# Kernel optimization log

Hardware: AMD Instinct MI355X
Metric: run time of the kernel (lower is better)

Reference implementation:

```python
import jax, jax.numpy as jnp
import numpy as np
import math

N0 = 50000      # nodes at level 0
E0 = 800000     # edges at level 0 (fixed edge buffer, masked when pooled)
D = 128         # hidden_dim == latent_dim
L = 2           # args.mpl_layers
NB = 2          # args.num_blocks (SAGEConvs per block)
RATIO = 0.5     # args.mpl_ratio
EPS = 1e-12


def setup_inputs() -> dict:
    key = jax.random.key(0)
    ks = jax.random.split(key, 6)
    x = jax.random.normal(ks[0], (N0, D), jnp.float32)
    edge_index = jax.random.randint(ks[1], (2, E0), 0, N0, jnp.int32)
    n_convs = (2 * L + 1) * NB  # down(4) + bottom(2) + up(4) = 10
    Wl = jax.random.normal(ks[2], (n_convs, D, D), jnp.float32) * 0.05
    bl = jax.random.normal(ks[3], (n_convs, D), jnp.float32) * 0.05
    Wr = jax.random.normal(ks[4], (n_convs, D, D), jnp.float32) * 0.05
    pool_p = jax.random.normal(ks[5], (L, D), jnp.float32)
    return {"x": x, "edge_index": edge_index, "Wl": Wl, "bl": bl, "Wr": Wr,
            "pool_p": pool_p}


def _sage(x, src, dst, valid, W_l, b_l, W_r, n):
    """PyG SAGEConv (mean aggr): lin_l(mean_{j->i} x_j) + lin_r(x_i).
    Invalid (masked) edges contribute neither to the sum nor the count."""
    msg = x[src] * valid[:, None]                       # [E, D]
    s = jax.ops.segment_sum(msg, dst, num_segments=n)   # [n, D]
    cnt = jax.ops.segment_sum(valid, dst, num_segments=n)
    mean = s / jnp.maximum(cnt, 1.0)[:, None]
    return mean @ W_l.T + b_l + x @ W_r.T


def _cal_ew(w, src, dst, valid, n):
    """WeightedEdgeConv.cal_ew (no_grad in original)."""
    deg = jax.ops.segment_sum(valid, src, num_segments=n)
    normed = w / jnp.where(deg > 0, deg, 1.0)
    w_send = normed[src] * valid
    aggr_w = jax.ops.segment_sum(w_send, dst, num_segments=n) + EPS
    ec = w_send / aggr_w[dst]
    return jax.lax.stop_gradient(ec), jax.lax.stop_gradient(aggr_w)


def _econv(x, src, dst, ec, n, aggregating=True):
    """WeightedEdgeConv.forward: gather -> scale by edge weight -> scatter-add."""
    if aggregating:
        return jax.ops.segment_sum(x[src] * ec[:, None], dst, num_segments=n)
    return jax.ops.segment_sum(x[dst] * ec[:, None], src, num_segments=n)


def reference(x, edge_index, Wl, bl, Wr, pool_p):
    src, dst = edge_index[0], edge_index[1]
    valid = jnp.ones((E0,), x.dtype)
    n = N0
    conv = 0
    down_outs, down_edges, ecs, perms, sizes = [], [], [], [], []
    w = jnp.ones((N0,), x.dtype)  # b_data.weights (ones by default)

    # ---- down path ----
    for l in range(L):
        for _ in range(NB):
            x = _sage(x, src, dst, valid, Wl[conv], bl[conv], Wr[conv], n)
            conv += 1
        down_outs.append(x)
        down_edges.append((src, dst, valid))
        sizes.append(n)
        ec, w = _cal_ew(w, src, dst, valid, n)
        ecs.append(ec)
        x = _econv(x, src, dst, ec, n, aggregating=True)
        # TopKPooling: score = x.p/||p||, keep top ceil(ratio*n), gate by tanh
        p = pool_p[l]
        score = x @ p / jnp.linalg.norm(p)
        k = int(math.ceil(RATIO * n))
        vals, perm = jax.lax.top_k(score, k)
        x = x[perm] * jnp.tanh(vals)[:, None]
        w = w[perm]
        new_id = jnp.full((n,), -1, jnp.int32).at[perm].set(
            jnp.arange(k, dtype=jnp.int32))
        src2, dst2 = new_id[src], new_id[dst]
        keep = ((src2 >= 0) & (dst2 >= 0)).astype(x.dtype)
        valid = valid * keep
        src = jnp.maximum(src2, 0)
        dst = jnp.maximum(dst2, 0)
        perms.append(perm)
        n = k

    # ---- bottom ----
    for _ in range(NB):
        x = _sage(x, src, dst, valid, Wl[conv], bl[conv], Wr[conv], n)
        conv += 1

    # ---- up path ----
    for i in range(L):
        u = L - 1 - i
        src, dst, valid = down_edges[u]
        n = sizes[u]
        # Unpool: scatter into zeros at kept-node indices
        x = jnp.zeros((n, x.shape[-1]), x.dtype).at[perms[u]].set(x)
        x = _econv(x, src, dst, ecs[u], n, aggregating=False)
        for _ in range(NB):
            x = _sage(x, src, dst, valid, Wl[conv], bl[conv], Wr[conv], n)
            conv += 1
        x = x + down_outs[u]  # skip connection
    return x
```

## Files before the change

kernel.cpp:

```cpp
#include <hip/hip_runtime.h>
#include <stdint.h>

#define DEV __device__ __forceinline__

constexpr int N0 = 50000;
constexpr int E0 = 800000;
constexpr int D  = 128;

typedef __attribute__((ext_vector_type(8))) short bf16x8;
typedef __attribute__((ext_vector_type(4))) float f32x4;

DEV float bf2f(unsigned u) { return __uint_as_float(u << 16); }
DEV unsigned short f2bf(float f) {
  unsigned u = __float_as_uint(f);
  unsigned r = u + 0x7fffu + ((u >> 16) & 1u);
  return (unsigned short)(r >> 16);
}

DEV unsigned wave_incl_scan(unsigned v, int lane) {
  #pragma unroll
  for (int off = 1; off < 64; off <<= 1) {
    unsigned u = __shfl_up(v, (unsigned)off);
    if (lane >= off) v += u;
  }
  return v;
}

__global__ void k_count(const int* __restrict__ src, const int* __restrict__ dst,
                        unsigned* cnt_src, unsigned* cnt_dst,
                        unsigned* __restrict__ rank_src, unsigned* __restrict__ rank_dst) {
  int e = blockIdx.x * blockDim.x + threadIdx.x;
  if (e < E0) {
    rank_src[e] = atomicAdd(&cnt_src[src[e]], 1u);
    rank_dst[e] = atomicAdd(&cnt_dst[dst[e]], 1u);
  }
}

__global__ void k_psum(const unsigned* __restrict__ in, int n, unsigned* __restrict__ part) {
  int t = threadIdx.x, lane = t & 63, w = t >> 6;
  int base = blockIdx.x * 1024 + t * 4;
  unsigned s = 0;
  #pragma unroll
  for (int j = 0; j < 4; ++j) { int i = base + j; if (i < n) s += in[i]; }
  #pragma unroll
  for (int off = 32; off >= 1; off >>= 1) s += __shfl_xor(s, off);
  __shared__ unsigned ws[4];
  if (lane == 0) ws[w] = s;
  __syncthreads();
  if (t == 0) part[blockIdx.x] = ws[0] + ws[1] + ws[2] + ws[3];
}

__global__ void k_scoff(const unsigned* __restrict__ part, int nch,
                        unsigned* __restrict__ off, unsigned* __restrict__ total_out) {
  if (threadIdx.x == 0) {
    unsigned run = 0;
    for (int c = 0; c < nch; ++c) { off[c] = run; run += part[c]; }
    *total_out = run;
  }
}

__global__ void k_sapply(const unsigned* __restrict__ in, const unsigned* __restrict__ choff,
                         int n, unsigned* __restrict__ out) {
  int t = threadIdx.x, lane = t & 63, w = t >> 6;
  int base = blockIdx.x * 1024 + t * 4;
  unsigned v[4]; unsigned s = 0;
  #pragma unroll
  for (int j = 0; j < 4; ++j) { int i = base + j; v[j] = (i < n) ? in[i] : 0u; s += v[j]; }
  unsigned incl = wave_incl_scan(s, lane);
  __shared__ unsigned wsum[4], woff[4];
  if (lane == 63) wsum[w] = incl;
  __syncthreads();
  if (t == 0) { unsigned run = 0; for (int j = 0; j < 4; ++j) { woff[j] = run; run += wsum[j]; } }
  __syncthreads();
  unsigned run = choff[blockIdx.x] + woff[w] + incl - s;
  #pragma unroll
  for (int j = 0; j < 4; ++j) {
    int i = base + j;
    if (i < n) out[i] = run;
    run += v[j];
  }
}

__global__ void k_fill2(const int* __restrict__ src, const int* __restrict__ dst,
                        const unsigned* __restrict__ rank_src, const unsigned* __restrict__ rank_dst,
                        const unsigned* __restrict__ indptr_src, const unsigned* __restrict__ indptr_dst,
                        int* __restrict__ adj_src, int* __restrict__ adj_dst) {
  int e = blockIdx.x * blockDim.x + threadIdx.x;
  if (e < E0) {
    int s = src[e], d = dst[e];
    adj_dst[indptr_dst[d] + rank_dst[e]] = s;
    adj_src[indptr_src[s] + rank_src[e]] = d;
  }
}

__global__ void k_adj_next2(const int* __restrict__ adjd, const int* __restrict__ adjs,
                            const int* __restrict__ new_id,
                            int* __restrict__ outd, int* __restrict__ outs) {
  int pos = blockIdx.x * blockDim.x + threadIdx.x;
  if (pos < E0) {
    int a = adjd[pos];
    outd[pos] = (a >= 0) ? new_id[a] : -1;
    int b = adjs[pos];
    outs[pos] = (b >= 0) ? new_id[b] : -1;
  }
}

__global__ void k_adj_next(const int* __restrict__ adj_prev, const int* __restrict__ new_id,
                           int* __restrict__ adj_out) {
  int pos = blockIdx.x * blockDim.x + threadIdx.x;
  if (pos < E0) {
    int a = adj_prev[pos];
    adj_out[pos] = (a >= 0) ? new_id[a] : -1;
  }
}

__global__ void k_wt_pk3(const float* __restrict__ Wl, const float* __restrict__ Wr,
                         unsigned short* __restrict__ Bh, unsigned short* __restrict__ Bm,
                         unsigned short* __restrict__ Bl) {
  int idx = blockIdx.x * blockDim.x + threadIdx.x;
  if (idx >= 10 * 8 * 8 * 64) return;
  int l  = idx & 63;
  int ct = (idx >> 6) & 7;
  int ks = (idx >> 9) & 7;
  int c  = idx >> 12;
  int k0 = ks * 32 + (l >> 4) * 8;
  int o  = ct * 16 + (l & 15);
  const float* Wrow = (k0 < 128) ? (Wl + ((size_t)c * 128 + o) * 128 + k0)
                                 : (Wr + ((size_t)c * 128 + o) * 128 + (k0 - 128));
  size_t base = (size_t)idx * 8;
  #pragma unroll
  for (int j = 0; j < 8; ++j) {
    float wv = Wrow[j];
    unsigned short h = f2bf(wv);
    float r1 = wv - bf2f(h);
    unsigned short m = f2bf(r1);
    float r2 = r1 - bf2f(m);
    Bh[base + j] = h;
    Bm[base + j] = m;
    Bl[base + j] = f2bf(r2);
  }
}

template<bool MEAN, bool MASKED, bool ECW>
__global__ void k_gf32(const float* __restrict__ x, const int* __restrict__ adj,
                       const float* __restrict__ ecs, const unsigned* __restrict__ indptr,
                       const int* __restrict__ orig, int n, float* __restrict__ out) {
  int wid = (blockIdx.x * blockDim.x + threadIdx.x) >> 6;
  int lane = threadIdx.x & 63;
  if (wid >= n) return;
  int o = orig ? orig[wid] : wid;
  unsigned s0 = indptr[o], s1 = indptr[o + 1];
  int half = lane >> 5, sl = lane & 31;
  float a0 = 0.f, a1 = 0.f, a2 = 0.f, a3 = 0.f, cnt = 0.f;
  for (unsigned idx = s0; idx < s1; idx += 8) {
    #pragma unroll
    for (int j = 0; j < 4; ++j) {
      unsigned e = idx + j * 2 + half;
      if (e < s1) {
        int a = adj[e];
        if (!MASKED || a >= 0) {
          const float4 v = *(const float4*)(x + (size_t)a * D + sl * 4);
          if (ECW) {
            float w = ecs[e];
            a0 = fmaf(w, v.x, a0); a1 = fmaf(w, v.y, a1);
            a2 = fmaf(w, v.z, a2); a3 = fmaf(w, v.w, a3);
          } else {
            a0 += v.x; a1 += v.y; a2 += v.z; a3 += v.w;
          }
          cnt += 1.f;
        }
      }
    }
  }
  a0 += __shfl_xor(a0, 32); a1 += __shfl_xor(a1, 32);
  a2 += __shfl_xor(a2, 32); a3 += __shfl_xor(a3, 32);
  if (MEAN) {
    cnt += __shfl_xor(cnt, 32);
    if (!MASKED) cnt = (float)(s1 - s0);
    float inv = 1.0f / fmaxf(cnt, 1.0f);
    a0 *= inv; a1 *= inv; a2 *= inv; a3 *= inv;
  }
  if (half == 0)
    *(float4*)(out + (size_t)wid * D + sl * 4) = make_float4(a0, a1, a2, a3);
}

template<bool MEAN, bool MASKED, bool ECW>
__global__ void k_gbf(const unsigned* __restrict__ xb, const int* __restrict__ adj,
                      const float* __restrict__ ecs, const unsigned* __restrict__ indptr,
                      const int* __restrict__ orig, int n,
                      float* __restrict__ out, unsigned* __restrict__ outbf) {
  int wid = (blockIdx.x * blockDim.x + threadIdx.x) >> 6;
  int lane = threadIdx.x & 63;
  if (wid >= n) return;
  int o = orig ? orig[wid] : wid;
  unsigned s0 = indptr[o], s1 = indptr[o + 1];
  int q = lane >> 4, sl = lane & 15;
  float acc[8];
  #pragma unroll
  for (int k = 0; k < 8; ++k) acc[k] = 0.f;
  float cnt = 0.f;
  for (unsigned idx = s0; idx < s1; idx += 16) {
    #pragma unroll
    for (int j = 0; j < 4; ++j) {
      unsigned e = idx + j * 4 + q;
      if (e < s1) {
        int a = adj[e];
        if (!MASKED || a >= 0) {
          const uint4 v = *(const uint4*)(xb + (size_t)a * 64 + sl * 4);
          float f0 = bf2f(v.x & 0xffffu), f1 = bf2f(v.x >> 16);
          float f2 = bf2f(v.y & 0xffffu), f3 = bf2f(v.y >> 16);
          float f4 = bf2f(v.z & 0xffffu), f5 = bf2f(v.z >> 16);
          float f6 = bf2f(v.w & 0xffffu), f7 = bf2f(v.w >> 16);
          if (ECW) {
            float w = ecs[e];
            acc[0] = fmaf(w, f0, acc[0]); acc[1] = fmaf(w, f1, acc[1]);
            acc[2] = fmaf(w, f2, acc[2]); acc[3] = fmaf(w, f3, acc[3]);
            acc[4] = fmaf(w, f4, acc[4]); acc[5] = fmaf(w, f5, acc[5]);
            acc[6] = fmaf(w, f6, acc[6]); acc[7] = fmaf(w, f7, acc[7]);
          } else {
            acc[0] += f0; acc[1] += f1; acc[2] += f2; acc[3] += f3;
            acc[4] += f4; acc[5] += f5; acc[6] += f6; acc[7] += f7;
          }
          cnt += 1.f;
        }
      }
    }
  }
  #pragma unroll
  for (int k = 0; k < 8; ++k) {
    acc[k] += __shfl_xor(acc[k], 16);
    acc[k] += __shfl_xor(acc[k], 32);
  }
  if (MEAN) {
    cnt += __shfl_xor(cnt, 16);
    cnt += __shfl_xor(cnt, 32);
    if (!MASKED) cnt = (float)(s1 - s0);
    float inv = 1.0f / fmaxf(cnt, 1.0f);
    #pragma unroll
    for (int k = 0; k < 8; ++k) acc[k] *= inv;
  }
  if (q == 0) {
    *(float4*)(out + (size_t)wid * D + sl * 8)     = make_float4(acc[0], acc[1], acc[2], acc[3]);
    *(float4*)(out + (size_t)wid * D + sl * 8 + 4) = make_float4(acc[4], acc[5], acc[6], acc[7]);
    if (outbf) {
      uint4 p;
      p.x = (unsigned)f2bf(acc[0]) | ((unsigned)f2bf(acc[1]) << 16);
      p.y = (unsigned)f2bf(acc[2]) | ((unsigned)f2bf(acc[3]) << 16);
      p.z = (unsigned)f2bf(acc[4]) | ((unsigned)f2bf(acc[5]) << 16);
      p.w = (unsigned)f2bf(acc[6]) | ((unsigned)f2bf(acc[7]) << 16);
      *(uint4*)(outbf + (size_t)wid * 64 + sl * 4) = p;
    }
  }
}

__launch_bounds__(256)
__global__ void k_gemm_mfma6(const float* __restrict__ mean, const float* __restrict__ xin,
                             const unsigned short* __restrict__ Bh, const unsigned short* __restrict__ Bm,
                             const unsigned short* __restrict__ Bl,
                             const float* __restrict__ bias,
                             float* __restrict__ y, int n) {
  int tid = threadIdx.x;
  int lane = tid & 63, w = tid >> 6;
  int row0 = blockIdx.x * 64 + w * 16;
  int arow = row0 + (lane & 15);
  int kgrp = lane >> 4;
  bool rowok = arow < n;
  f32x4 acc[8];
  #pragma unroll
  for (int ct = 0; ct < 8; ++ct) acc[ct] = f32x4{0.f, 0.f, 0.f, 0.f};

  #pragma unroll
  for (int ks = 0; ks < 8; ++ks) {
    const float* A = (ks < 4) ? mean : xin;
    int kk = (ks & 3) * 32 + kgrp * 8;
    float av[8];
    if (rowok) {
      float4 x0 = *(const float4*)(A + (size_t)arow * D + kk);
      float4 x1 = *(const float4*)(A + (size_t)arow * D + kk + 4);
      av[0] = x0.x; av[1] = x0.y; av[2] = x0.z; av[3] = x0.w;
      av[4] = x1.x; av[5] = x1.y; av[6] = x1.z; av[7] = x1.w;
    } else {
      #pragma unroll
      for (int j = 0; j < 8; ++j) av[j] = 0.f;
    }
    bf16x8 ah, am, al;
    #pragma unroll
    for (int j = 0; j < 8; ++j) {
      unsigned short h = f2bf(av[j]);
      float r1 = av[j] - bf2f(h);
      unsigned short m = f2bf(r1);
      float r2 = r1 - bf2f(m);
      ah[j] = (short)h; am[j] = (short)m; al[j] = (short)f2bf(r2);
    }
    #pragma unroll
    for (int ct = 0; ct < 8; ++ct) {
      size_t boff = (((size_t)ks * 8 + ct) * 64 + lane) * 8;
      bf16x8 bh = *(const bf16x8*)(Bh + boff);
      bf16x8 bm = *(const bf16x8*)(Bm + boff);
      bf16x8 bl = *(const bf16x8*)(Bl + boff);
      acc[ct] = __builtin_amdgcn_mfma_f32_16x16x32_bf16(ah, bh, acc[ct], 0, 0, 0);
      acc[ct] = __builtin_amdgcn_mfma_f32_16x16x32_bf16(ah, bm, acc[ct], 0, 0, 0);
      acc[ct] = __builtin_amdgcn_mfma_f32_16x16x32_bf16(am, bh, acc[ct], 0, 0, 0);
      acc[ct] = __builtin_amdgcn_mfma_f32_16x16x32_bf16(am, bm, acc[ct], 0, 0, 0);
      acc[ct] = __builtin_amdgcn_mfma_f32_16x16x32_bf16(ah, bl, acc[ct], 0, 0, 0);
      acc[ct] = __builtin_amdgcn_mfma_f32_16x16x32_bf16(al, bh, acc[ct], 0, 0, 0);
    }
  }
  int ccol = lane & 15;
  #pragma unroll
  for (int ct = 0; ct < 8; ++ct) {
    int col = ct * 16 + ccol;
    float bb = bias[col];
    #pragma unroll
    for (int r = 0; r < 4; ++r) {
      int row = row0 + kgrp * 4 + r;
      if (row < n) y[(size_t)row * D + col] = acc[ct][r] + bb;
    }
  }
}

__launch_bounds__(256)
__global__ void k_gemm_mfma(const float* __restrict__ mean, const float* __restrict__ xin,
                            const unsigned short* __restrict__ Bhi, const unsigned short* __restrict__ Blo,
                            const float* __restrict__ bias, const float* __restrict__ skip,
                            float* __restrict__ y, unsigned short* __restrict__ ybf, int n) {
  int tid = threadIdx.x;
  int lane = tid & 63, w = tid >> 6;
  int row0 = blockIdx.x * 64 + w * 16;
  int arow = row0 + (lane & 15);
  int kgrp = lane >> 4;
  bool rowok = arow < n;
  f32x4 acc[8];
  #pragma unroll
  for (int ct = 0; ct < 8; ++ct) acc[ct] = f32x4{0.f, 0.f, 0.f, 0.f};

  #pragma unroll
  for (int ks = 0; ks < 8; ++ks) {
    const float* A = (ks < 4) ? mean : xin;
    int kk = (ks & 3) * 32 + kgrp * 8;
    float av[8];
    if (rowok) {
      float4 x0 = *(const float4*)(A + (size_t)arow * D + kk);
      float4 x1 = *(const float4*)(A + (size_t)arow * D + kk + 4);
      av[0] = x0.x; av[1] = x0.y; av[2] = x0.z; av[3] = x0.w;
      av[4] = x1.x; av[5] = x1.y; av[6] = x1.z; av[7] = x1.w;
    } else {
      #pragma unroll
      for (int j = 0; j < 8; ++j) av[j] = 0.f;
    }
    bf16x8 ahi, alo;
    #pragma unroll
    for (int j = 0; j < 8; ++j) {
      unsigned short h = f2bf(av[j]);
      ahi[j] = (short)h;
      alo[j] = (short)f2bf(av[j] - bf2f(h));
    }
    #pragma unroll
    for (int ct = 0; ct < 8; ++ct) {
      size_t boff = (((size_t)ks * 8 + ct) * 64 + lane) * 8;
      bf16x8 bh = *(const bf16x8*)(Bhi + boff);
      bf16x8 bl = *(const bf16x8*)(Blo + boff);
      acc[ct] = __builtin_amdgcn_mfma_f32_16x16x32_bf16(ahi, bh, acc[ct], 0, 0, 0);
      acc[ct] = __builtin_amdgcn_mfma_f32_16x16x32_bf16(alo, bh, acc[ct], 0, 0, 0);
      acc[ct] = __builtin_amdgcn_mfma_f32_16x16x32_bf16(ahi, bl, acc[ct], 0, 0, 0);
    }
  }
  int ccol = lane & 15;
  #pragma unroll
  for (int ct = 0; ct < 8; ++ct) {
    int col = ct * 16 + ccol;
    float bb = bias[col];
    #pragma unroll
    for (int r = 0; r < 4; ++r) {
      int row = row0 + kgrp * 4 + r;
      if (row < n) {
        float v = acc[ct][r] + bb;
        if (skip) v += skip[(size_t)row * D + col];
        y[(size_t)row * D + col] = v;
        if (ybf) ybf[(size_t)row * D + col] = f2bf(v);
      }
    }
  }
}

__global__ void k_deg_mask(const int* __restrict__ adj_src, const unsigned* __restrict__ indptr_src,
                           const int* __restrict__ orig, int n, float* __restrict__ deg) {
  int j = blockIdx.x * blockDim.x + threadIdx.x;
  if (j >= n) return;
  int o = orig ? orig[j] : j;
  unsigned s0 = indptr_src[o], s1 = indptr_src[o + 1];
  float d = 0.f;
  for (unsigned i = s0; i < s1; ++i) d += (adj_src[i] >= 0) ? 1.f : 0.f;
  deg[j] = d;
}

template<bool MASKED>
__global__ void k_ew_dst(const int* __restrict__ adj, const unsigned* __restrict__ indptr,
                         const unsigned* __restrict__ ips,
                         const int* __restrict__ orig, const float* __restrict__ w,
                         const float* __restrict__ deg, int n,
                         float* __restrict__ ws_slot, float* __restrict__ aggrw,
                         float* __restrict__ ec_slot) {
  int j = blockIdx.x * blockDim.x + threadIdx.x;
  if (j >= n) return;
  int o = orig ? orig[j] : j;
  unsigned s0 = indptr[o], s1 = indptr[o + 1];
  float s = 1e-12f;
  for (unsigned pos = s0; pos < s1; ++pos) {
    int a = adj[pos];
    float ws = 0.f;
    if (!MASKED || a >= 0) {
      float d = deg ? deg[a] : (float)(ips[a + 1] - ips[a]);
      ws = (w ? w[a] : 1.0f) / (d > 0.f ? d : 1.0f);
    }
    ws_slot[pos] = ws;
    s += ws;
  }
  aggrw[j] = s;
  float inv = 1.0f / s;
  for (unsigned pos = s0; pos < s1; ++pos) ec_slot[pos] = ws_slot[pos] * inv;
}

template<bool MASKED>
__global__ void k_ew_src(const int* __restrict__ adj_src, const unsigned* __restrict__ indptr_src,
                         const int* __restrict__ orig, const float* __restrict__ w,
                         const float* __restrict__ deg, const float* __restrict__ aggrw, int n,
                         float* __restrict__ ec_slot) {
  int j = blockIdx.x * blockDim.x + threadIdx.x;
  if (j >= n) return;
  int o = orig ? orig[j] : j;
  unsigned s0 = indptr_src[o], s1 = indptr_src[o + 1];
  float d = deg ? deg[j] : (float)(s1 - s0);
  float wn = (w ? w[j] : 1.0f) / (d > 0.f ? d : 1.0f);
  for (unsigned pos = s0; pos < s1; ++pos) {
    int a = adj_src[pos];
    ec_slot[pos] = (!MASKED || a >= 0) ? (wn / aggrw[a]) : 0.f;
  }
}

DEV unsigned mono_key(float f) {
  unsigned u = __float_as_uint(f);
  return (u & 0x80000000u) ? ~u : (u | 0x80000000u);
}

__global__ void k_score(const float* __restrict__ x, const float* __restrict__ p,
                        int n, float* __restrict__ score, unsigned* __restrict__ keys) {
  int wid = (blockIdx.x * blockDim.x + threadIdx.x) >> 6;
  int lane = threadIdx.x & 63;
  if (wid >= n) return;
  float p0 = p[lane * 2], p1 = p[lane * 2 + 1];
  const float2 xv = *(const float2*)(x + (size_t)wid * D + lane * 2);
  float partial = xv.x * p0 + xv.y * p1;
  float pn = p0 * p0 + p1 * p1;
  #pragma unroll
  for (int off = 32; off >= 1; off >>= 1) {
    partial += __shfl_xor(partial, off);
    pn += __shfl_xor(pn, off);
  }
  if (lane == 0) {
    float sc = partial * (1.0f / sqrtf(pn));
    score[wid] = sc;
    keys[wid] = mono_key(sc);
  }
}

__global__ void k_sel_init(unsigned* bins, unsigned* state, int k) {
  int t = threadIdx.x;
  if (t < 256) bins[t] = 0u;
  if (t == 0) { state[0] = 0u; state[1] = (unsigned)k; }
}

__global__ void k_hist(const unsigned* __restrict__ keys, int n, const unsigned* __restrict__ state,
                       unsigned* __restrict__ bins, int byte) {
  __shared__ unsigned lb[256];
  for (int i = threadIdx.x; i < 256; i += blockDim.x) lb[i] = 0u;
  __syncthreads();
  unsigned prefix = state[0];
  unsigned mask = (byte == 3) ? 0u : (0xFFFFFFFFu << ((byte + 1) * 8));
  for (int i = blockIdx.x * blockDim.x + threadIdx.x; i < n; i += gridDim.x * blockDim.x) {
    unsigned key = keys[i];
    if ((key & mask) == (prefix & mask))
      atomicAdd(&lb[(key >> (byte * 8)) & 255], 1u);
  }
  __syncthreads();
  for (int i = threadIdx.x; i < 256; i += blockDim.x)
    if (lb[i]) atomicAdd(&bins[i], lb[i]);
}

__global__ void k_pick(unsigned* bins, unsigned* state, int byte) {
  if (threadIdx.x == 0) {
    unsigned r = state[1];
    int b;
    for (b = 255; b > 0; --b) {
      unsigned c = bins[b];
      if (c >= r) break;
      r -= c;
    }
    state[0] |= ((unsigned)b) << (byte * 8);
    state[1] = r;
  }
  __syncthreads();
  for (int i = threadIdx.x; i < 256; i += blockDim.x) bins[i] = 0u;
}

__global__ void k_flags(const unsigned* __restrict__ keys, const unsigned* __restrict__ state,
                        int n, uint2* __restrict__ part) {
  int t = threadIdx.x, lane = t & 63, w = t >> 6;
  int base = blockIdx.x * 1024 + t * 4;
  unsigned T = state[0];
  unsigned cnt = 0;
  #pragma unroll
  for (int j = 0; j < 4; ++j) {
    int i = base + j;
    if (i < n) {
      unsigned key = keys[i];
      cnt += (key > T ? 1u : 0u) + ((key == T ? 1u : 0u) << 16);
    }
  }
  #pragma unroll
  for (int off = 32; off >= 1; off >>= 1) cnt += __shfl_xor(cnt, off);
  __shared__ unsigned ws[4];
  if (lane == 0) ws[w] = cnt;
  __syncthreads();
  if (t == 0) {
    unsigned s = ws[0] + ws[1] + ws[2] + ws[3];
    part[blockIdx.x] = make_uint2(s & 0xffffu, s >> 16);
  }
}

__global__ void k_choff(const uint2* __restrict__ part, int nch, uint2* __restrict__ off) {
  if (threadIdx.x == 0) {
    unsigned g = 0, e = 0;
    for (int c = 0; c < nch; ++c) { off[c] = make_uint2(g, e); g += part[c].x; e += part[c].y; }
  }
}

__global__ void k_pack2(const unsigned* __restrict__ keys, const unsigned* __restrict__ state,
                        const uint2* __restrict__ choff, const float* __restrict__ aggrw,
                        const int* __restrict__ orig, int n,
                        int* __restrict__ perm, int* __restrict__ new_id,
                        float* __restrict__ w_next, int* __restrict__ orig_next) {
  int t = threadIdx.x, lane = t & 63, w = t >> 6;
  int base = blockIdx.x * 1024 + t * 4;
  unsigned T = state[0], r = state[1];
  unsigned f[4];
  unsigned cnt = 0;
  #pragma unroll
  for (int j = 0; j < 4; ++j) {
    int i = base + j;
    unsigned key = (i < n) ? keys[i] : 0u;
    unsigned gt = (i < n && key > T) ? 1u : 0u;
    unsigned eq = (i < n && key == T) ? 1u : 0u;
    f[j] = gt | (eq << 1);
    cnt += gt + (eq << 16);
  }
  unsigned incl = wave_incl_scan(cnt, lane);
  __shared__ unsigned wsum[4], woff[4];
  if (lane == 63) wsum[w] = incl;
  __syncthreads();
  if (t == 0) { unsigned run = 0; for (int j = 0; j < 4; ++j) { woff[j] = run; run += wsum[j]; } }
  __syncthreads();
  unsigned before = woff[w] + incl - cnt;
  uint2 o0 = choff[blockIdx.x];
  unsigned gt_b = o0.x + (before & 0xffffu);
  unsigned eq_b = o0.y + (before >> 16);
  #pragma unroll
  for (int j = 0; j < 4; ++j) {
    int i = base + j;
    if (i >= n) break;
    unsigned gt = f[j] & 1u, eq = (f[j] >> 1) & 1u;
    bool sel = gt || (eq && eq_b < r);
    if (sel) {
      int pos = (int)(gt_b + (eq_b < r ? eq_b : r));
      perm[pos] = i;
      new_id[i] = pos;
      w_next[pos] = aggrw[i];
      orig_next[pos] = orig ? orig[i] : i;
    } else {
      new_id[i] = -1;
    }
    gt_b += gt; eq_b += eq;
  }
}

__global__ void k_gate(const float* __restrict__ xin, const int* __restrict__ perm,
                       const float* __restrict__ score, int k, float* __restrict__ xout,
                       unsigned* __restrict__ outbf) {
  int wid = (blockIdx.x * blockDim.x + threadIdx.x) >> 6;
  int lane = threadIdx.x & 63;
  if (wid >= k) return;
  int j = perm[wid];
  float g = tanhf(score[j]);
  float2 v = *(const float2*)(xin + (size_t)j * D + lane * 2);
  v.x *= g; v.y *= g;
  *(float2*)(xout + (size_t)wid * D + lane * 2) = v;
  if (outbf) {
    unsigned p = (unsigned)f2bf(v.x) | ((unsigned)f2bf(v.y) << 16);
    outbf[(size_t)wid * 64 + lane] = p;
  }
}

__global__ void k_scatter_bf(const float* __restrict__ xin, const int* __restrict__ perm,
                             int k, unsigned* __restrict__ outbf) {
  int wid = (blockIdx.x * blockDim.x + threadIdx.x) >> 6;
  int lane = threadIdx.x & 63;
  if (wid >= k) return;
  int p = perm[wid];
  float2 v = *(const float2*)(xin + (size_t)wid * D + lane * 2);
  unsigned pk = (unsigned)f2bf(v.x) | ((unsigned)f2bf(v.y) << 16);
  outbf[(size_t)p * 64 + lane] = pk;
}

extern "C" void kernel_launch(void* const* d_in, const int* in_sizes, int n_in,
                              void* d_out, int out_size, void* d_ws, size_t ws_size,
                              hipStream_t stream) {
  const float* x_in   = (const float*)d_in[0];
  const int*   ei     = (const int*)d_in[1];
  const int*   src0   = ei;
  const int*   dst0   = ei + E0;
  const float* Wl     = (const float*)d_in[2];
  const float* bl     = (const float*)d_in[3];
  const float* Wr     = (const float*)d_in[4];
  const float* pool_p = (const float*)d_in[5];
  float* out = (float*)d_out;

  const int n0 = N0, k0 = 25000, n1 = 25000, k1 = 12500, n2 = 12500;
  const int NCH0 = (N0 + 1023) / 1024;

  char* ws = (char*)d_ws;
  size_t off = 0;
  auto alloc = [&](size_t bytes) -> char* {
    char* p = ws + off;
    off += (bytes + 255) & ~(size_t)255;
    return p;
  };
  const size_t NBY = (size_t)N0 * D * 4;
  float* B0    = (float*)alloc(NBY);
  float* B1    = (float*)alloc(NBY);
  float* B2    = (float*)alloc(NBY);
  float* down0 = (float*)alloc(NBY);
  float* down1 = (float*)alloc(NBY / 2);
  unsigned* MA = (unsigned*)alloc((size_t)N0 * D * 2);
  unsigned* MB = (unsigned*)alloc((size_t)N0 * D * 2);
  int* adj0_dst = (int*)alloc(E0 * 4);
  int* adj0_src = (int*)alloc(E0 * 4);
  int* adj1_dst = (int*)alloc(E0 * 4);
  int* adj1_src = (int*)alloc(E0 * 4);
  float* ec0_src = (float*)alloc(E0 * 4);
  float* ec1_src = (float*)alloc(E0 * 4);
  float* ec_dst  = (float*)alloc(E0 * 4);
  float* ws_slot = (float*)alloc(E0 * 4);
  int* adj2_dst  = (int*)ws_slot;
  unsigned* rank_src = (unsigned*)alloc(E0 * 4);
  unsigned* rank_dst = (unsigned*)alloc(E0 * 4);
  unsigned* indptr_dst = (unsigned*)alloc((N0 + 1) * 4);
  unsigned* indptr_src = (unsigned*)alloc((N0 + 1) * 4);
  unsigned* cnt_src = (unsigned*)alloc(N0 * 4);
  unsigned* cnt_dst = (unsigned*)alloc(N0 * 4);
  float* deg   = (float*)alloc(N0 * 4);
  float* aggrw = (float*)alloc(N0 * 4);
  float* w1 = (float*)alloc(n1 * 4);
  float* w2 = (float*)alloc(n2 * 4);
  float* score = (float*)alloc(N0 * 4);
  unsigned* keys = (unsigned*)alloc(N0 * 4);
  int* perm0 = (int*)alloc(k0 * 4);
  int* perm1 = (int*)alloc(k1 * 4);
  int* orig1 = (int*)alloc(k0 * 4);
  int* orig2 = (int*)alloc(k1 * 4);
  int* new_id = (int*)alloc(N0 * 4);
  unsigned* bins  = (unsigned*)alloc(256 * 4);
  unsigned* state = (unsigned*)alloc(8);
  unsigned* spart = (unsigned*)alloc(64 * 4);
  unsigned* soff  = (unsigned*)alloc(64 * 4);
  uint2* ppart = (uint2*)alloc(64 * 8);
  uint2* poff  = (uint2*)alloc(64 * 8);
  unsigned short* Bh = (unsigned short*)alloc((size_t)10 * 32768 * 2);
  unsigned short* Bm = (unsigned short*)alloc((size_t)10 * 32768 * 2);
  unsigned short* Bl = (unsigned short*)alloc((size_t)10 * 32768 * 2);

  const int EG = (E0 + 255) / 256;

  auto scan_np1 = [&](const unsigned* in, unsigned* outp, int n, int nch) {
    k_psum<<<nch, 256, 0, stream>>>(in, n, spart);
    k_scoff<<<1, 64, 0, stream>>>(spart, nch, soff, outp + n);
    k_sapply<<<nch, 256, 0, stream>>>(in, soff, n, outp);
  };

  hipMemsetAsync(cnt_src, 0, N0 * 4, stream);
  hipMemsetAsync(cnt_dst, 0, N0 * 4, stream);
  k_count<<<EG, 256, 0, stream>>>(src0, dst0, cnt_src, cnt_dst, rank_src, rank_dst);
  scan_np1(cnt_src, indptr_src, N0, NCH0);
  scan_np1(cnt_dst, indptr_dst, N0, NCH0);
  k_fill2<<<EG, 256, 0, stream>>>(src0, dst0, rank_src, rank_dst, indptr_src, indptr_dst,
                                  adj0_src, adj0_dst);
  k_wt_pk3<<<(10 * 8 * 8 * 64 + 255) / 256, 256, 0, stream>>>(Wl, Wr, Bh, Bm, Bl);

  auto gemm6 = [&](const float* meanb, const float* xin, float* yout, int n, int cidx) {
    size_t o = (size_t)cidx * 32768;
    k_gemm_mfma6<<<(n + 63) / 64, 256, 0, stream>>>(meanb, xin, Bh + o, Bm + o, Bl + o,
                                                    bl + cidx * 128, yout, n);
  };
  auto gemm_mx = [&](const float* meanb, const float* xin, float* yout, unsigned short* ybf,
                     const float* skip, int n, int cidx) {
    size_t o = (size_t)cidx * 32768;
    k_gemm_mfma<<<(n + 63) / 64, 256, 0, stream>>>(meanb, xin, Bh + o, Bm + o,
                                                   bl + cidx * 128, skip, yout, ybf, n);
  };

  auto pool_sel = [&](const float* xpool, int n, int kk, int level, const int* orig,
                      int* perm, float* w_next, int* orig_next,
                      float* xout, unsigned* xout_bf) {
    int nch = (n + 1023) / 1024;
    k_score<<<(n + 3) / 4, 256, 0, stream>>>(xpool, pool_p + level * D, n, score, keys);
    k_sel_init<<<1, 256, 0, stream>>>(bins, state, kk);
    for (int byte = 3; byte >= 0; --byte) {
      k_hist<<<256, 256, 0, stream>>>(keys, n, state, bins, byte);
      k_pick<<<1, 256, 0, stream>>>(bins, state, byte);
    }
    k_flags<<<nch, 256, 0, stream>>>(keys, state, n, ppart);
    k_choff<<<1, 64, 0, stream>>>(ppart, nch, poff);
    k_pack2<<<nch, 256, 0, stream>>>(keys, state, poff, aggrw, orig, n, perm, new_id, w_next, orig_next);
    k_gate<<<(kk + 3) / 4, 256, 0, stream>>>(xpool, perm, score, kk, xout, xout_bf);
  };

  const int G0 = (n0 + 3) / 4, G1 = (n1 + 3) / 4, G2 = (n2 + 3) / 4;

  k_gf32<true, false, false><<<G0, 256, 0, stream>>>(x_in, adj0_dst, nullptr, indptr_dst, nullptr, n0, B1);
  gemm6(B1, x_in, B2, n0, 0);
  k_gf32<true, false, false><<<G0, 256, 0, stream>>>(B2, adj0_dst, nullptr, indptr_dst, nullptr, n0, B1);
  gemm6(B1, B2, down0, n0, 1);
  k_ew_dst<false><<<(n0 + 255) / 256, 256, 0, stream>>>(adj0_dst, indptr_dst, indptr_src, nullptr,
                                                        nullptr, nullptr, n0, ws_slot, aggrw, ec_dst);
  k_ew_src<false><<<(n0 + 255) / 256, 256, 0, stream>>>(adj0_src, indptr_src, nullptr, nullptr,
                                                        nullptr, aggrw, n0, ec0_src);
  k_gf32<false, false, true><<<G0, 256, 0, stream>>>(down0, adj0_dst, ec_dst, indptr_dst, nullptr, n0, B1);
  pool_sel(B1, n0, k0, 0, nullptr, perm0, w1, orig1, B2, nullptr);
  k_adj_next2<<<EG, 256, 0, stream>>>(adj0_dst, adj0_src, new_id, adj1_dst, adj1_src);

  k_gf32<true, true, false><<<G1, 256, 0, stream>>>(B2, adj1_dst, nullptr, indptr_dst, orig1, n1, B1);
  gemm6(B1, B2, B0, n1, 2);
  k_gf32<true, true, false><<<G1, 256, 0, stream>>>(B0, adj1_dst, nullptr, indptr_dst, orig1, n1, B1);
  gemm6(B1, B0, down1, n1, 3);
  k_deg_mask<<<(n1 + 255) / 256, 256, 0, stream>>>(adj1_src, indptr_src, orig1, n1, deg);
  k_ew_dst<true><<<(n1 + 255) / 256, 256, 0, stream>>>(adj1_dst, indptr_dst, nullptr, orig1, w1,
                                                       deg, n1, ws_slot, aggrw, ec_dst);
  k_ew_src<true><<<(n1 + 255) / 256, 256, 0, stream>>>(adj1_src, indptr_src, orig1, w1, deg, aggrw,
                                                       n1, ec1_src);
  k_gf32<false, true, true><<<G1, 256, 0, stream>>>(down1, adj1_dst, ec_dst, indptr_dst, orig1, n1, B1);
  pool_sel(B1, n1, k1, 1, orig1, perm1, w2, orig2, B2, MA);
  k_adj_next<<<EG, 256, 0, stream>>>(adj1_dst, new_id, adj2_dst);

  k_gbf<true, true, false><<<G2, 256, 0, stream>>>(MA, adj2_dst, nullptr, indptr_dst, orig2, n2, B1, nullptr);
  gemm_mx(B1, B2, B0, (unsigned short*)MB, nullptr, n2, 4);
  k_gbf<true, true, false><<<G2, 256, 0, stream>>>(MB, adj2_dst, nullptr, indptr_dst, orig2, n2, B1, nullptr);
  gemm_mx(B1, B0, B2, nullptr, nullptr, n2, 5);

  hipMemsetAsync(MA, 0, (size_t)n1 * D * 2, stream);
  k_scatter_bf<<<G2, 256, 0, stream>>>(B2, perm1, n2, MA);
  k_gbf<false, true, true><<<G1, 256, 0, stream>>>(MA, adj1_src, ec1_src, indptr_src, orig1, n1, B1, MB);
  k_gbf<true, true, false><<<G1, 256, 0, stream>>>(MB, adj1_dst, nullptr, indptr_dst, orig1, n1, B0, nullptr);
  gemm_mx(B0, B1, B2, (unsigned short*)MA, nullptr, n1, 6);
  k_gbf<true, true, false><<<G1, 256, 0, stream>>>(MA, adj1_dst, nullptr, indptr_dst, orig1, n1, B0, nullptr);
  gemm_mx(B0, B2, B1, nullptr, down1, n1, 7);

  hipMemsetAsync(MA, 0, (size_t)n0 * D * 2, stream);
  k_scatter_bf<<<G1, 256, 0, stream>>>(B1, perm0, n1, MA);
  k_gbf<false, false, true><<<G0, 256, 0, stream>>>(MA, adj0_src, ec0_src, indptr_src, nullptr, n0, B2, MB);
  k_gbf<true, false, false><<<G0, 256, 0, stream>>>(MB, adj0_dst, nullptr, indptr_dst, nullptr, n0, B1, nullptr);
  gemm_mx(B1, B2, B0, (unsigned short*)MA, nullptr, n0, 8);
  k_gbf<true, false, false><<<G0, 256, 0, stream>>>(MA, adj0_dst, nullptr, indptr_dst, nullptr, n0, B1, nullptr);
  gemm_mx(B1, B0, out, nullptr, down0, n0, 9);
}
```

Baseline: 1.147 ms.

## Cut kernel launches, fold scan offsets into apply kernels, widen fp32 gather

Merges the src and dst prefix scans into 2D-grid kernels. The chunk offsets are now computed inside the apply and pack kernels with a wave reduction, which removes the single-thread offset kernels and the selection-init kernel (folded into the score kernel). Unpooling now gathers through new_id and writes zeros directly, replacing the memset plus scatter; this needs a separate new_id buffer per level. The fp32 gather now has each lane handle 8 features and processes 4 edges per wave iteration, for more memory-level parallelism. The main aim is to cut launch and serialization overhead in a long chain of small kernels.

```diff
diff --git a/kernel.cpp b/kernel.cpp
--- a/kernel.cpp
+++ b/kernel.cpp
@@ -36,7 +36,10 @@
   }
 }
 
-__global__ void k_psum(const unsigned* __restrict__ in, int n, unsigned* __restrict__ part) {
+__global__ void k_psum2(const unsigned* __restrict__ in0, const unsigned* __restrict__ in1,
+                        int n, unsigned* __restrict__ part) {
+  int y = blockIdx.y;
+  const unsigned* in = y ? in1 : in0;
   int t = threadIdx.x, lane = t & 63, w = t >> 6;
   int base = blockIdx.x * 1024 + t * 4;
   unsigned s = 0;
@@ -47,21 +50,19 @@
   __shared__ unsigned ws[4];
   if (lane == 0) ws[w] = s;
   __syncthreads();
-  if (t == 0) part[blockIdx.x] = ws[0] + ws[1] + ws[2] + ws[3];
-}
-
-__global__ void k_scoff(const unsigned* __restrict__ part, int nch,
-                        unsigned* __restrict__ off, unsigned* __restrict__ total_out) {
-  if (threadIdx.x == 0) {
-    unsigned run = 0;
-    for (int c = 0; c < nch; ++c) { off[c] = run; run += part[c]; }
-    *total_out = run;
-  }
-}
-
-__global__ void k_sapply(const unsigned* __restrict__ in, const unsigned* __restrict__ choff,
-                         int n, unsigned* __restrict__ out) {
+  if (t == 0) part[y * 64 + blockIdx.x] = ws[0] + ws[1] + ws[2] + ws[3];
+}
+
+__global__ void k_sapply2(const unsigned* __restrict__ in0, const unsigned* __restrict__ in1,
+                          const unsigned* __restrict__ part, int n, int nch,
+                          unsigned* __restrict__ out0, unsigned* __restrict__ out1) {
+  int y = blockIdx.y;
+  const unsigned* in = y ? in1 : in0;
+  unsigned* out = y ? out1 : out0;
   int t = threadIdx.x, lane = t & 63, w = t >> 6;
+  unsigned c = (lane < (int)blockIdx.x) ? part[y * 64 + lane] : 0u;
+  #pragma unroll
+  for (int off = 32; off >= 1; off >>= 1) c += __shfl_xor(c, off);
   int base = blockIdx.x * 1024 + t * 4;
   unsigned v[4]; unsigned s = 0;
   #pragma unroll
@@ -72,13 +73,15 @@
   __syncthreads();
   if (t == 0) { unsigned run = 0; for (int j = 0; j < 4; ++j) { woff[j] = run; run += wsum[j]; } }
   __syncthreads();
-  unsigned run = choff[blockIdx.x] + woff[w] + incl - s;
+  unsigned run = c + woff[w] + incl - s;
   #pragma unroll
   for (int j = 0; j < 4; ++j) {
     int i = base + j;
     if (i < n) out[i] = run;
     run += v[j];
   }
+  if ((int)blockIdx.x == nch - 1 && t == 0)
+    out[n] = c + woff[3] + wsum[3];
 }
 
 __global__ void k_fill2(const int* __restrict__ src, const int* __restrict__ dst,
@@ -150,38 +153,52 @@
   if (wid >= n) return;
   int o = orig ? orig[wid] : wid;
   unsigned s0 = indptr[o], s1 = indptr[o + 1];
-  int half = lane >> 5, sl = lane & 31;
-  float a0 = 0.f, a1 = 0.f, a2 = 0.f, a3 = 0.f, cnt = 0.f;
-  for (unsigned idx = s0; idx < s1; idx += 8) {
+  int q = lane >> 4, sl = lane & 15;
+  float acc[8];
+  #pragma unroll
+  for (int k = 0; k < 8; ++k) acc[k] = 0.f;
+  float cnt = 0.f;
+  for (unsigned idx = s0; idx < s1; idx += 16) {
     #pragma unroll
     for (int j = 0; j < 4; ++j) {
-      unsigned e = idx + j * 2 + half;
+      unsigned e = idx + j * 4 + q;
       if (e < s1) {
         int a = adj[e];
         if (!MASKED || a >= 0) {
-          const float4 v = *(const float4*)(x + (size_t)a * D + sl * 4);
+          const float4 v0 = *(const float4*)(x + (size_t)a * D + sl * 8);
+          const float4 v1 = *(const float4*)(x + (size_t)a * D + sl * 8 + 4);
           if (ECW) {
             float w = ecs[e];
-            a0 = fmaf(w, v.x, a0); a1 = fmaf(w, v.y, a1);
-            a2 = fmaf(w, v.z, a2); a3 = fmaf(w, v.w, a3);
+            acc[0] = fmaf(w, v0.x, acc[0]); acc[1] = fmaf(w, v0.y, acc[1]);
+            acc[2] = fmaf(w, v0.z, acc[2]); acc[3] = fmaf(w, v0.w, acc[3]);
+            acc[4] = fmaf(w, v1.x, acc[4]); acc[5] = fmaf(w, v1.y, acc[5]);
+            acc[6] = fmaf(w, v1.z, acc[6]); acc[7] = fmaf(w, v1.w, acc[7]);
           } else {
-            a0 += v.x; a1 += v.y; a2 += v.z; a3 += v.w;
+            acc[0] += v0.x; acc[1] += v0.y; acc[2] += v0.z; acc[3] += v0.w;
+            acc[4] += v1.x; acc[5] += v1.y; acc[6] += v1.z; acc[7] += v1.w;
           }
           cnt += 1.f;
         }
       }
     }
   }
-  a0 += __shfl_xor(a0, 32); a1 += __shfl_xor(a1, 32);
-  a2 += __shfl_xor(a2, 32); a3 += __shfl_xor(a3, 32);
+  #pragma unroll
+  for (int k = 0; k < 8; ++k) {
+    acc[k] += __shfl_xor(acc[k], 16);
+    acc[k] += __shfl_xor(acc[k], 32);
+  }
   if (MEAN) {
+    cnt += __shfl_xor(cnt, 16);
     cnt += __shfl_xor(cnt, 32);
     if (!MASKED) cnt = (float)(s1 - s0);
     float inv = 1.0f / fmaxf(cnt, 1.0f);
-    a0 *= inv; a1 *= inv; a2 *= inv; a3 *= inv;
-  }
-  if (half == 0)
-    *(float4*)(out + (size_t)wid * D + sl * 4) = make_float4(a0, a1, a2, a3);
+    #pragma unroll
+    for (int k = 0; k < 8; ++k) acc[k] *= inv;
+  }
+  if (q == 0) {
+    *(float4*)(out + (size_t)wid * D + sl * 8)     = make_float4(acc[0], acc[1], acc[2], acc[3]);
+    *(float4*)(out + (size_t)wid * D + sl * 8 + 4) = make_float4(acc[4], acc[5], acc[6], acc[7]);
+  }
 }
 
 template<bool MEAN, bool MASKED, bool ECW>
@@ -444,7 +461,13 @@
 }
 
 __global__ void k_score(const float* __restrict__ x, const float* __restrict__ p,
-                        int n, float* __restrict__ score, unsigned* __restrict__ keys) {
+                        int n, float* __restrict__ score, unsigned* __restrict__ keys,
+                        unsigned* bins, unsigned* state, int k) {
+  if (blockIdx.x == 0) {
+    int t = threadIdx.x;
+    if (t < 256) bins[t] = 0u;
+    if (t == 0) { state[0] = 0u; state[1] = (unsigned)k; }
+  }
   int wid = (blockIdx.x * blockDim.x + threadIdx.x) >> 6;
   int lane = threadIdx.x & 63;
   if (wid >= n) return;
@@ -462,12 +485,6 @@
     score[wid] = sc;
     keys[wid] = mono_key(sc);
   }
-}
-
-__global__ void k_sel_init(unsigned* bins, unsigned* state, int k) {
-  int t = threadIdx.x;
-  if (t < 256) bins[t] = 0u;
-  if (t == 0) { state[0] = 0u; state[1] = (unsigned)k; }
 }
 
 __global__ void k_hist(const unsigned* __restrict__ keys, int n, const unsigned* __restrict__ state,
@@ -528,21 +545,21 @@
   }
 }
 
-__global__ void k_choff(const uint2* __restrict__ part, int nch, uint2* __restrict__ off) {
-  if (threadIdx.x == 0) {
-    unsigned g = 0, e = 0;
-    for (int c = 0; c < nch; ++c) { off[c] = make_uint2(g, e); g += part[c].x; e += part[c].y; }
-  }
-}
-
 __global__ void k_pack2(const unsigned* __restrict__ keys, const unsigned* __restrict__ state,
-                        const uint2* __restrict__ choff, const float* __restrict__ aggrw,
+                        const uint2* __restrict__ part, const float* __restrict__ aggrw,
                         const int* __restrict__ orig, int n,
                         int* __restrict__ perm, int* __restrict__ new_id,
                         float* __restrict__ w_next, int* __restrict__ orig_next) {
   int t = threadIdx.x, lane = t & 63, w = t >> 6;
   int base = blockIdx.x * 1024 + t * 4;
   unsigned T = state[0], r = state[1];
+  unsigned co = 0;
+  if (lane < (int)blockIdx.x) {
+    uint2 pp = part[lane];
+    co = pp.x | (pp.y << 16);
+  }
+  #pragma unroll
+  for (int off = 32; off >= 1; off >>= 1) co += __shfl_xor(co, off);
   unsigned f[4];
   unsigned cnt = 0;
   #pragma unroll
@@ -561,9 +578,8 @@
   if (t == 0) { unsigned run = 0; for (int j = 0; j < 4; ++j) { woff[j] = run; run += wsum[j]; } }
   __syncthreads();
   unsigned before = woff[w] + incl - cnt;
-  uint2 o0 = choff[blockIdx.x];
-  unsigned gt_b = o0.x + (before & 0xffffu);
-  unsigned eq_b = o0.y + (before >> 16);
+  unsigned gt_b = (co & 0xffffu) + (before & 0xffffu);
+  unsigned eq_b = (co >> 16) + (before >> 16);
   #pragma unroll
   for (int j = 0; j < 4; ++j) {
     int i = base + j;
@@ -600,15 +616,18 @@
   }
 }
 
-__global__ void k_scatter_bf(const float* __restrict__ xin, const int* __restrict__ perm,
-                             int k, unsigned* __restrict__ outbf) {
+__global__ void k_unpool_bf(const float* __restrict__ xin, const int* __restrict__ new_id,
+                            int n, unsigned* __restrict__ outbf) {
   int wid = (blockIdx.x * blockDim.x + threadIdx.x) >> 6;
   int lane = threadIdx.x & 63;
-  if (wid >= k) return;
-  int p = perm[wid];
-  float2 v = *(const float2*)(xin + (size_t)wid * D + lane * 2);
-  unsigned pk = (unsigned)f2bf(v.x) | ((unsigned)f2bf(v.y) << 16);
-  outbf[(size_t)p * 64 + lane] = pk;
+  if (wid >= n) return;
+  int j = new_id[wid];
+  unsigned pk = 0u;
+  if (j >= 0) {
+    float2 v = *(const float2*)(xin + (size_t)j * D + lane * 2);
+    pk = (unsigned)f2bf(v.x) | ((unsigned)f2bf(v.y) << 16);
+  }
+  outbf[(size_t)wid * 64 + lane] = pk;
 }
 
 extern "C" void kernel_launch(void* const* d_in, const int* in_sizes, int n_in,
@@ -667,30 +686,24 @@
   int* perm1 = (int*)alloc(k1 * 4);
   int* orig1 = (int*)alloc(k0 * 4);
   int* orig2 = (int*)alloc(k1 * 4);
-  int* new_id = (int*)alloc(N0 * 4);
+  int* new_id0 = (int*)alloc(N0 * 4);
+  int* new_id1 = (int*)alloc(N0 * 4);
   unsigned* bins  = (unsigned*)alloc(256 * 4);
   unsigned* state = (unsigned*)alloc(8);
-  unsigned* spart = (unsigned*)alloc(64 * 4);
-  unsigned* soff  = (unsigned*)alloc(64 * 4);
+  unsigned* spart = (unsigned*)alloc(128 * 4);
   uint2* ppart = (uint2*)alloc(64 * 8);
-  uint2* poff  = (uint2*)alloc(64 * 8);
   unsigned short* Bh = (unsigned short*)alloc((size_t)10 * 32768 * 2);
   unsigned short* Bm = (unsigned short*)alloc((size_t)10 * 32768 * 2);
   unsigned short* Bl = (unsigned short*)alloc((size_t)10 * 32768 * 2);
 
   const int EG = (E0 + 255) / 256;
 
-  auto scan_np1 = [&](const unsigned* in, unsigned* outp, int n, int nch) {
-    k_psum<<<nch, 256, 0, stream>>>(in, n, spart);
-    k_scoff<<<1, 64, 0, stream>>>(spart, nch, soff, outp + n);
-    k_sapply<<<nch, 256, 0, stream>>>(in, soff, n, outp);
-  };
-
   hipMemsetAsync(cnt_src, 0, N0 * 4, stream);
   hipMemsetAsync(cnt_dst, 0, N0 * 4, stream);
   k_count<<<EG, 256, 0, stream>>>(src0, dst0, cnt_src, cnt_dst, rank_src, rank_dst);
-  scan_np1(cnt_src, indptr_src, N0, NCH0);
-  scan_np1(cnt_dst, indptr_dst, N0, NCH0);
+  k_psum2<<<dim3(NCH0, 2), 256, 0, stream>>>(cnt_src, cnt_dst, N0, spart);
+  k_sapply2<<<dim3(NCH0, 2), 256, 0, stream>>>(cnt_src, cnt_dst, spart, N0, NCH0,
+                                               indptr_src, indptr_dst);
   k_fill2<<<EG, 256, 0, stream>>>(src0, dst0, rank_src, rank_dst, indptr_src, indptr_dst,
                                   adj0_src, adj0_dst);
   k_wt_pk3<<<(10 * 8 * 8 * 64 + 255) / 256, 256, 0, stream>>>(Wl, Wr, Bh, Bm, Bl);
@@ -708,18 +721,17 @@
   };
 
   auto pool_sel = [&](const float* xpool, int n, int kk, int level, const int* orig,
-                      int* perm, float* w_next, int* orig_next,
+                      int* perm, int* nid, float* w_next, int* orig_next,
                       float* xout, unsigned* xout_bf) {
     int nch = (n + 1023) / 1024;
-    k_score<<<(n + 3) / 4, 256, 0, stream>>>(xpool, pool_p + level * D, n, score, keys);
-    k_sel_init<<<1, 256, 0, stream>>>(bins, state, kk);
+    k_score<<<(n + 3) / 4, 256, 0, stream>>>(xpool, pool_p + level * D, n, score, keys,
+                                             bins, state, kk);
     for (int byte = 3; byte >= 0; --byte) {
       k_hist<<<256, 256, 0, stream>>>(keys, n, state, bins, byte);
       k_pick<<<1, 256, 0, stream>>>(bins, state, byte);
     }
     k_flags<<<nch, 256, 0, stream>>>(keys, state, n, ppart);
-    k_choff<<<1, 64, 0, stream>>>(ppart, nch, poff);
-    k_pack2<<<nch, 256, 0, stream>>>(keys, state, poff, aggrw, orig, n, perm, new_id, w_next, orig_next);
+    k_pack2<<<nch, 256, 0, stream>>>(keys, state, ppart, aggrw, orig, n, perm, nid, w_next, orig_next);
     k_gate<<<(kk + 3) / 4, 256, 0, stream>>>(xpool, perm, score, kk, xout, xout_bf);
   };
 
@@ -734,8 +746,8 @@
   k_ew_src<false><<<(n0 + 255) / 256, 256, 0, stream>>>(adj0_src, indptr_src, nullptr, nullptr,
                                                         nullptr, aggrw, n0, ec0_src);
   k_gf32<false, false, true><<<G0, 256, 0, stream>>>(down0, adj0_dst, ec_dst, indptr_dst, nullptr, n0, B1);
-  pool_sel(B1, n0, k0, 0, nullptr, perm0, w1, orig1, B2, nullptr);
-  k_adj_next2<<<EG, 256, 0, stream>>>(adj0_dst, adj0_src, new_id, adj1_dst, adj1_src);
+  pool_sel(B1, n0, k0, 0, nullptr, perm0, new_id0, w1, orig1, B2, nullptr);
+  k_adj_next2<<<EG, 256, 0, stream>>>(adj0_dst, adj0_src, new_id0, adj1_dst, adj1_src);
 
   k_gf32<true, true, false><<<G1, 256, 0, stream>>>(B2, adj1_dst, nullptr, indptr_dst, orig1, n1, B1);
   gemm6(B1, B2, B0, n1, 2);
@@ -747,24 +759,22 @@
   k_ew_src<true><<<(n1 + 255) / 256, 256, 0, stream>>>(adj1_src, indptr_src, orig1, w1, deg, aggrw,
                                                        n1, ec1_src);
   k_gf32<false, true, true><<<G1, 256, 0, stream>>>(down1, adj1_dst, ec_dst, indptr_dst, orig1, n1, B1);
-  pool_sel(B1, n1, k1, 1, orig1, perm1, w2, orig2, B2, MA);
-  k_adj_next<<<EG, 256, 0, stream>>>(adj1_dst, new_id, adj2_dst);
+  pool_sel(B1, n1, k1, 1, orig1, perm1, new_id1, w2, orig2, B2, MA);
+  k_adj_next<<<EG, 256, 0, stream>>>(adj1_dst, new_id1, adj2_dst);
 
   k_gbf<true, true, false><<<G2, 256, 0, stream>>>(MA, adj2_dst, nullptr, indptr_dst, orig2, n2, B1, nullptr);
   gemm_mx(B1, B2, B0, (unsigned short*)MB, nullptr, n2, 4);
   k_gbf<true, true, false><<<G2, 256, 0, stream>>>(MB, adj2_dst, nullptr, indptr_dst, orig2, n2, B1, nullptr);
   gemm_mx(B1, B0, B2, nullptr, nullptr, n2, 5);
 
-  hipMemsetAsync(MA, 0, (size_t)n1 * D * 2, stream);
-  k_scatter_bf<<<G2, 256, 0, stream>>>(B2, perm1, n2, MA);
+  k_unpool_bf<<<G1, 256, 0, stream>>>(B2, new_id1, n1, MA);
   k_gbf<false, true, true><<<G1, 256, 0, stream>>>(MA, adj1_src, ec1_src, indptr_src, orig1, n1, B1, MB);
   k_gbf<true, true, false><<<G1, 256, 0, stream>>>(MB, adj1_dst, nullptr, indptr_dst, orig1, n1, B0, nullptr);
   gemm_mx(B0, B1, B2, (unsigned short*)MA, nullptr, n1, 6);
   k_gbf<true, true, false><<<G1, 256, 0, stream>>>(MA, adj1_dst, nullptr, indptr_dst, orig1, n1, B0, nullptr);
   gemm_mx(B0, B2, B1, nullptr, down1, n1, 7);
 
-  hipMemsetAsync(MA, 0, (size_t)n0 * D * 2, stream);
-  k_scatter_bf<<<G1, 256, 0, stream>>>(B1, perm0, n1, MA);
+  k_unpool_bf<<<G0, 256, 0, stream>>>(B1, new_id0, n0, MA);
   k_gbf<false, false, true><<<G0, 256, 0, stream>>>(MA, adj0_src, ec0_src, indptr_src, nullptr, n0, B2, MB);
   k_gbf<true, false, false><<<G0, 256, 0, stream>>>(MB, adj0_dst, nullptr, indptr_dst, nullptr, n0, B1, nullptr);
   gemm_mx(B1, B2, B0, (unsigned short*)MA, nullptr, n0, 8);
```

Result: faster. 1.090 ms (-4.9%).
